# Kernel optimization log

Hardware: AMD Instinct MI355X
Metric: run time of the kernel (lower is better)

The kernel has to match this reference:

```python
import jax, jax.numpy as jnp
import numpy as np

# ---- quantization constants (8-bit, per-tensor affine; representative values) ----
Q_MAX = 255.0
S_IN, Z_IN = 0.05, 128.0      # block input
S1, Z1 = 0.04, 128.0          # after expand 1x1 + hardswish
S2, Z2 = 0.04, 128.0          # after depthwise 5x5 + hardswish
S_SE1, Z_SE1 = 0.03, 128.0    # SE fc1 output
S_SE2, Z_SE2 = 1.0 / 255.0, 0.0  # SE fc2 hardsigmoid output in [0,1]
S_MUL, Z_MUL = 0.04, 128.0    # SE gated activation
S3, Z3 = 0.05, 128.0          # after project 1x1
S_OUT, Z_OUT = 0.06, 128.0    # after residual add
W_SCALE = 0.01                # symmetric per-tensor weight scale (zero_point = 0)
EXP_C = 576                   # expanded channels (depthwise groups)


def conv(x, w, stride=1, padding=0, groups=1):
    return jax.lax.conv_general_dilated(
        x, w, (stride, stride), [(padding, padding), (padding, padding)],
        feature_group_count=groups, dimension_numbers=('NCHW', 'OIHW', 'NCHW'))


def hardswish(x):
    return x * jnp.clip(x + 3.0, 0.0, 6.0) * (1.0 / 6.0)


def hardsigmoid(x):
    return jnp.clip(x + 3.0, 0.0, 6.0) * (1.0 / 6.0)


def qconv(x_q, w_q, b_q, s_in, z_in, s_out, z_out, stride=1, padding=0, groups=1, act=None):
    """Quantized conv: int-domain accumulation (simulated in fp32), fused activation
    on the dequantized accumulator, then requantize to [0, Q_MAX]."""
    acc = conv(x_q - z_in, w_q, stride, padding, groups) + b_q[None, :, None, None]
    deq = acc * (s_in * W_SCALE)  # dequantize accumulator
    if act == 'hardswish':
        deq = hardswish(deq)
    elif act == 'hardsigmoid':
        deq = hardsigmoid(deq)
    return jnp.clip(deq * (1.0 / s_out) + z_out, 0.0, Q_MAX)


def setup_inputs() -> dict:
    key = jax.random.key(0)
    ks = jax.random.split(key, 11)
    def qw(k, shape):  # int8-style symmetric weights stored as fp32 integers
        return jnp.round(jnp.clip(jax.random.normal(k, shape) * 40.0, -127.0, 127.0))
    def qb(k, n):      # int32-style bias in accumulator domain
        return jnp.round(jax.random.normal(k, (n,)) * 500.0)
    return {
        'x':      jnp.round(jax.random.uniform(ks[0], (64, 96, 28, 28)) * Q_MAX),
        'w_exp':  qw(ks[1], (576, 96, 1, 1)),  'b_exp':  qb(ks[2], 576),
        'w_dw':   qw(ks[3], (576, 1, 5, 5)),   'b_dw':   qb(ks[4], 576),
        'w_se1':  qw(ks[5], (144, 576, 1, 1)), 'b_se1':  qb(ks[6], 144),
        'w_se2':  qw(ks[7], (576, 144, 1, 1)), 'b_se2':  qb(ks[8], 576),
        'w_proj': qw(ks[9], (96, 576, 1, 1)),  'b_proj': qb(ks[10], 96),
    }


def reference(x, w_exp, b_exp, w_dw, b_dw, w_se1, b_se1, w_se2, b_se2, w_proj, b_proj):
    # expand 1x1 (+ hardswish)
    e = qconv(x, w_exp, b_exp, S_IN, Z_IN, S1, Z1, act='hardswish')
    # depthwise 5x5, padding=(5-1)//2=2, groups=expanded (+ hardswish)
    d = qconv(e, w_dw, b_dw, S1, Z1, S2, Z2, padding=2, groups=EXP_C, act='hardswish')
    # squeeze-excitation: global avg pool -> fc1 -> fc2(hardsigmoid) -> quantized mul
    pooled = jnp.mean(d, axis=(2, 3), keepdims=True)  # [N, 576, 1, 1]
    g1 = qconv(pooled, w_se1, b_se1, S2, Z2, S_SE1, Z_SE1)
    g2 = qconv(g1, w_se2, b_se2, S_SE1, Z_SE1, S_SE2, Z_SE2, act='hardsigmoid')
    gated = jnp.clip((g2 - Z_SE2) * (d - Z2) * (S_SE2 * S2 / S_MUL) + Z_MUL, 0.0, Q_MAX)
    # project 1x1 (linear)
    p = qconv(gated, w_proj, b_proj, S_MUL, Z_MUL, S3, Z3)
    # quantized residual add (stride=1, in==out channels -> use_res_connect)
    out = jnp.clip((x - Z_IN) * (S_IN / S_OUT) + (p - Z3) * (S3 / S_OUT) + Z_OUT, 0.0, Q_MAX)
    return out
```

## Files before the change

### kernel.cpp

```cpp
#include <hip/hip_runtime.h>

typedef _Float16 v8h __attribute__((ext_vector_type(8)));
typedef _Float16 v4h __attribute__((ext_vector_type(4)));
typedef _Float16 v2h __attribute__((ext_vector_type(2)));
typedef float v4f __attribute__((ext_vector_type(4)));

#define NB 64
#define CI 96
#define CE 576
#define CO 96
#define HW 784
#define SEC 144

#if defined(__has_builtin)
#if __has_builtin(__builtin_amdgcn_fdot2)
#define HAVE_FDOT2 1
#endif
#endif

__device__ __forceinline__ float fdot2(v2h a, v2h b, float c) {
#ifdef HAVE_FDOT2
  return __builtin_amdgcn_fdot2(a, b, c, false);
#else
  return (float)a[0] * (float)b[0] + ((float)a[1] * (float)b[1] + c);
#endif
}

__global__ __launch_bounds__(256) void k0x_pack(const float* __restrict__ x,
                                                const float* __restrict__ w_exp,
                                                const float* __restrict__ w_proj,
                                                _Float16* __restrict__ x_f,
                                                _Float16* __restrict__ x_h,
                                                _Float16* __restrict__ w_exp_h,
                                                _Float16* __restrict__ w_proj_h) {
  __shared__ _Float16 xl[112][104];
  const int tid = threadIdx.x;
  const int n = blockIdx.y;
  const int hw0 = blockIdx.x * 112;

  if (n == 0) {
    for (int i = blockIdx.x * 256 + tid; i < CE * CI; i += 7 * 256) {
      w_exp_h[i]  = (_Float16)w_exp[i];
      w_proj_h[i] = (_Float16)w_proj[i];
    }
  }

  for (int idx = tid; idx < CI * 28; idx += 256) {
    int c = idx / 28, seg = idx % 28;
    const float4 v = *(const float4*)&x[(n * CI + c) * HW + hw0 + seg * 4];
    int row = seg * 4;
    v4h xh;
    xh[0] = (_Float16)(v.x - 128.0f);
    xh[1] = (_Float16)(v.y - 128.0f);
    xh[2] = (_Float16)(v.z - 128.0f);
    xh[3] = (_Float16)(v.w - 128.0f);
    xl[row + 0][c] = xh[0];
    xl[row + 1][c] = xh[1];
    xl[row + 2][c] = xh[2];
    xl[row + 3][c] = xh[3];
    *(v4h*)&x_h[(n * CI + c) * HW + hw0 + seg * 4] = xh;
  }
  __syncthreads();

  for (int idx = tid; idx < 1344; idx += 256) {
    int t_l = idx / 192, rem = idx % 192, s = rem / 64, ln = rem % 64;
    int hw_l = t_l * 16 + (ln & 15), ci = s * 32 + (ln >> 4) * 8;
    v8h o;
#pragma unroll
    for (int j = 0; j < 8; ++j) o[j] = xl[hw_l][ci + j];
    size_t t = (size_t)(blockIdx.x * 7 + t_l);
    *(v8h*)&x_f[(((size_t)n * 49 + t) * 3 + s) * 512 + ln * 8] = o;
  }
}

__global__ __launch_bounds__(512, 8) void k12_fused(const _Float16* __restrict__ x_f,
                                                    const _Float16* __restrict__ w_exp_h,
                                                    const float* __restrict__ b_exp,
                                                    const float* __restrict__ w_dw,
                                                    const float* __restrict__ b_dw,
                                                    _Float16* __restrict__ d_t,
                                                    float* __restrict__ d_sums2) {
  __shared__ _Float16 e_lds[16][18][42];
  __shared__ _Float16 d_tile[16][392];
  __shared__ _Float16 w_pairs[16][5][8];
  const int tid = threadIdx.x;
  const int n = blockIdx.z;
  const int h = blockIdx.y;
  const int c0 = blockIdx.x * 16;

  {
    unsigned long long* z = (unsigned long long*)&e_lds[0][0][0];
    for (int idx = tid; idx < 16 * 18 * 42 * 2 / 8; idx += 512) z[idx] = 0ull;
  }
  for (int idx = tid; idx < 640; idx += 512) {
    int c = idx / 40, r = idx % 40, dy = r / 8, k = r % 8;
    int tap = (k < 4) ? k : (k - 3);
    w_pairs[c][dy][k] = (_Float16)w_dw[(c0 + c) * 25 + dy * 5 + tap];
  }
  __syncthreads();

  const int wv = tid >> 6, lane = tid & 63;
  const int l15 = lane & 15, q = lane >> 4;

  {
    const _Float16* wrow = &w_exp_h[(c0 + l15) * CI + q * 8];
    v8h b0 = *(const v8h*)(wrow);
    v8h b1 = *(const v8h*)(wrow + 32);
    v8h b2 = *(const v8h*)(wrow + 64);
    const float bia = b_exp[c0 + l15];

    const int ir0 = 14 * h - 2;
    const _Float16* xb = x_f + (size_t)n * (49 * 3 * 512) + lane * 8;
    for (int t_l = wv; t_l < 28; t_l += 8) {
      int t = 21 * h + t_l;
      const _Float16* xt = xb + (size_t)t * (3 * 512);
      v8h a0 = *(const v8h*)(xt);
      v8h a1 = *(const v8h*)(xt + 512);
      v8h a2 = *(const v8h*)(xt + 1024);
      v4f acc = (v4f){0.f, 0.f, 0.f, 0.f};
      acc = __builtin_amdgcn_mfma_f32_16x16x32_f16(a0, b0, acc, 0, 0, 0);
      acc = __builtin_amdgcn_mfma_f32_16x16x32_f16(a1, b1, acc, 0, 0, 0);
      acc = __builtin_amdgcn_mfma_f32_16x16x32_f16(a2, b2, acc, 0, 0, 0);
      int p = t * 16 + q * 4;
      int y = p / 28, xx = p - y * 28;
      int r_l = y - ir0;
      v4h ev;
#pragma unroll
      for (int r = 0; r < 4; ++r) {
        float deq = (acc[r] + bia) * 5.0e-4f;
        float cl  = fminf(fmaxf(deq + 3.0f, 0.0f), 6.0f);
        float evf = fminf(fmaxf(deq * cl * (25.0f / 6.0f), -128.0f), 127.0f);
        ev[r] = (_Float16)evf;
      }
      *(v4h*)&e_lds[l15][r_l][8 + xx] = ev;
    }
  }
  __syncthreads();

  const int c = tid >> 5, l = tid & 31;
  v2h W01[5], W23[5], W12[5], W34[5];
  float W0s[5], W4s[5];
#pragma unroll
  for (int dy = 0; dy < 5; ++dy) {
    W01[dy] = *(const v2h*)&w_pairs[c][dy][0];
    W23[dy] = *(const v2h*)&w_pairs[c][dy][2];
    W12[dy] = *(const v2h*)&w_pairs[c][dy][4];
    W34[dy] = *(const v2h*)&w_pairs[c][dy][6];
    W0s[dy] = (float)W01[dy][0];
    W4s[dy] = (float)W34[dy][1];
  }
  const float bc = b_dw[c0 + c];

  float csum = 0.0f;
  if (l < 28) {
    const int ry = l >> 1;
    const int bx = (l & 1) * 14;
    v2h P0[5], P1[5], P2[5], P3[5];
#pragma unroll
    for (int dy = 0; dy < 5; ++dy) {
      const _Float16* row = &e_lds[c][ry + dy][bx];
      P0[dy] = *(const v2h*)(row + 6);
      P1[dy] = *(const v2h*)(row + 8);
      P2[dy] = *(const v2h*)(row + 10);
      P3[dy] = *(const v2h*)(row + 12);
    }
#pragma unroll
    for (int xi = 0; xi < 3; ++xi) {
      const int x0 = bx + xi * 4;
      float o0 = bc, o1 = bc, o2 = bc, o3 = bc;
#pragma unroll
      for (int dy = 0; dy < 5; ++dy) {
        o0 = fdot2(P0[dy], W01[dy], o0);
        o0 = fdot2(P1[dy], W23[dy], o0);
        o0 += (float)P2[dy][0] * W4s[dy];
        o1 += (float)P0[dy][1] * W0s[dy];
        o1 = fdot2(P1[dy], W12[dy], o1);
        o1 = fdot2(P2[dy], W34[dy], o1);
        o2 = fdot2(P1[dy], W01[dy], o2);
        o2 = fdot2(P2[dy], W23[dy], o2);
        o2 += (float)P3[dy][0] * W4s[dy];
        o3 += (float)P1[dy][1] * W0s[dy];
        o3 = fdot2(P2[dy], W12[dy], o3);
        o3 = fdot2(P3[dy], W34[dy], o3);
      }
      float oo[4] = {o0, o1, o2, o3};
      v2h dva, dvb;
#pragma unroll
      for (int i = 0; i < 4; ++i) {
        float deq = oo[i] * 4.0e-4f;
        float cl  = fminf(fmaxf(deq + 3.0f, 0.0f), 6.0f);
        float dvv = fminf(fmaxf(deq * cl * (25.0f / 6.0f), -128.0f), 127.0f);
        if (i < 2) dva[i] = (_Float16)dvv; else dvb[i - 2] = (_Float16)dvv;
        csum += dvv;
      }
      *(v2h*)&d_tile[c][ry * 28 + x0]     = dva;
      *(v2h*)&d_tile[c][ry * 28 + x0 + 2] = dvb;
#pragma unroll
      for (int dy = 0; dy < 5; ++dy) {
        const _Float16* row = &e_lds[c][ry + dy][bx];
        P0[dy] = P2[dy];
        P1[dy] = P3[dy];
        P2[dy] = *(const v2h*)(row + x0 - bx + 14);
        P3[dy] = *(const v2h*)(row + x0 - bx + 16);
      }
    }
    {
      float o0 = bc, o1 = bc;
#pragma unroll
      for (int dy = 0; dy < 5; ++dy) {
        o0 = fdot2(P0[dy], W01[dy], o0);
        o0 = fdot2(P1[dy], W23[dy], o0);
        o0 += (float)P2[dy][0] * W4s[dy];
        o1 += (float)P0[dy][1] * W0s[dy];
        o1 = fdot2(P1[dy], W12[dy], o1);
        o1 = fdot2(P2[dy], W34[dy], o1);
      }
      v2h dv;
      float oo[2] = {o0, o1};
#pragma unroll
      for (int i = 0; i < 2; ++i) {
        float deq = oo[i] * 4.0e-4f;
        float cl  = fminf(fmaxf(deq + 3.0f, 0.0f), 6.0f);
        float dvv = fminf(fmaxf(deq * cl * (25.0f / 6.0f), -128.0f), 127.0f);
        dv[i] = (_Float16)dvv;
        csum += dvv;
      }
      *(v2h*)&d_tile[c][ry * 28 + bx + 12] = dv;
    }
  }
#pragma unroll
  for (int m = 16; m >= 1; m >>= 1) csum += __shfl_xor(csum, m);
  if (l == 0) d_sums2[((size_t)h * NB + n) * CE + c0 + c] = csum;

  __syncthreads();
  const size_t obase = ((size_t)n * 72 + (c0 >> 3)) * 784 + 392 * h;
  if (tid < 392) {
    int hw_l = tid;
    v8h o0, o1;
#pragma unroll
    for (int j = 0; j < 8; ++j) { o0[j] = d_tile[j][hw_l]; o1[j] = d_tile[8 + j][hw_l]; }
    *(v8h*)&d_t[(obase + hw_l) * 8] = o0;
    *(v8h*)&d_t[(obase + 784 + hw_l) * 8] = o1;
  }
}

__global__ __launch_bounds__(256) void k3a_fc1(const float* __restrict__ d_sums2,
                                               const float* __restrict__ w_se1,
                                               const float* __restrict__ b_se1,
                                               float* __restrict__ g1) {
  const int tid = threadIdx.x;
  const int wv = tid >> 6, lane = tid & 63;
  const int n = blockIdx.y;
  const int o = blockIdx.x * 4 + wv;
  const float* wrow = &w_se1[o * CE];
  const float* s0 = &d_sums2[(size_t)n * CE];
  const float* s1 = &d_sums2[((size_t)NB + n) * CE];
  float p = 0.f;
#pragma unroll
  for (int s = 0; s < 9; ++s) {
    int cc = lane + s * 64;
    p += wrow[cc] * (s0[cc] + s1[cc]);
  }
#pragma unroll
  for (int m = 32; m >= 1; m >>= 1) p += __shfl_xor(p, m);
  if (lane == 0) {
    float deq = (p * (1.0f / 784.0f) + b_se1[o]) * 4.0e-4f;
    g1[n * SEC + o] = fminf(fmaxf(deq * 33.3333333f + 128.0f, 0.0f), 255.0f) - 128.0f;
  }
}

__global__ __launch_bounds__(256) void k3b_fc2(const float* __restrict__ g1,
                                               const float* __restrict__ w_se2,
                                               const float* __restrict__ b_se2,
                                               _Float16* __restrict__ g2h) {
  const int tid = threadIdx.x;
  const int wv = tid >> 6, lane = tid & 63;
  const int n = blockIdx.y;
  const int o = blockIdx.x * 4 + wv;
  const float* wrow = &w_se2[o * SEC];
  const float* grow = &g1[n * SEC];
  float p = wrow[lane] * grow[lane] + wrow[lane + 64] * grow[lane + 64];
  if (lane < 16) p += wrow[lane + 128] * grow[lane + 128];
#pragma unroll
  for (int m = 32; m >= 1; m >>= 1) p += __shfl_xor(p, m);
  if (lane == 0) {
    float deq = (p + b_se2[o]) * 3.0e-4f;
    g2h[n * CE + o] =
        (_Float16)(fminf(fmaxf(deq + 3.0f, 0.0f), 6.0f) * (1.0f / 6.0f));
  }
}

__global__ __launch_bounds__(192) void k4_proj(const _Float16* __restrict__ d_t,
                                               const _Float16* __restrict__ g2h,
                                               const _Float16* __restrict__ w_proj_h,
                                               const float* __restrict__ b_proj,
                                               const _Float16* __restrict__ x_h,
                                               float* __restrict__ out) {
  const int tid = threadIdx.x;
  const int n = blockIdx.z;
  const int co0 = blockIdx.y * 48;
  const int hw0 = blockIdx.x * 112;
  const int wv = tid >> 6, lane = tid & 63;
  const int l15 = lane & 15, q = lane >> 4;

  v4f acc[7];
#pragma unroll
  for (int t = 0; t < 7; ++t) acc[t] = (v4f){0.f, 0.f, 0.f, 0.f};

  const _Float16* dbase = d_t + (((size_t)n * 72 + q) * 784 + hw0 + l15) * 8;
  const _Float16* abase = &w_proj_h[(co0 + wv * 16 + l15) * CE + q * 8];
  const _Float16* gbase = &g2h[(size_t)n * CE + q * 8];

  for (int ks = 0; ks < 18; ++ks) {
    v8h a = *(const v8h*)(abase + ks * 32);
    v8h g = *(const v8h*)(gbase + ks * 32);
    v8h ag = a * g;
    const _Float16* dk = dbase + (size_t)ks * (4 * 784 * 8);
#pragma unroll
    for (int t = 0; t < 7; ++t) {
      v8h b = *(const v8h*)(dk + t * (16 * 8));
      acc[t] = __builtin_amdgcn_mfma_f32_16x16x32_f16(ag, b, acc[t], 0, 0, 0);
    }
  }

  float bia[4];
#pragma unroll
  for (int r = 0; r < 4; ++r) bia[r] = b_proj[co0 + wv * 16 + q * 4 + r];

#pragma unroll
  for (int t = 0; t < 7; ++t) {
#pragma unroll
    for (int r = 0; r < 4; ++r) {
      int co = co0 + wv * 16 + q * 4 + r;
      int hw = hw0 + t * 16 + l15;
      float p = fminf(fmaxf((acc[t][r] + bia[r]) * 4.0e-4f * 20.0f + 128.0f, 0.0f), 255.0f);
      float xv = (float)x_h[(n * CO + co) * HW + hw];
      float o = xv * 0.8333333333f + (p - 128.0f) * 0.8333333333f + 128.0f;
      out[(n * CO + co) * HW + hw] = fminf(fmaxf(o, 0.0f), 255.0f);
    }
  }
}

extern "C" void kernel_launch(void* const* d_in, const int* in_sizes, int n_in,
                              void* d_out, int out_size, void* d_ws, size_t ws_size,
                              hipStream_t stream) {
  const float* x      = (const float*)d_in[0];
  const float* w_exp  = (const float*)d_in[1];
  const float* b_exp  = (const float*)d_in[2];
  const float* w_dw   = (const float*)d_in[3];
  const float* b_dw   = (const float*)d_in[4];
  const float* w_se1  = (const float*)d_in[5];
  const float* b_se1  = (const float*)d_in[6];
  const float* w_se2  = (const float*)d_in[7];
  const float* b_se2  = (const float*)d_in[8];
  const float* w_proj = (const float*)d_in[9];
  const float* b_proj = (const float*)d_in[10];
  float* out = (float*)d_out;

  char* ws = (char*)d_ws;
  const size_t SZ_W  = (size_t)CE * CI * 2;
  const size_t SZ_XF = (size_t)NB * 49 * 3 * 512 * 2;
  const size_t SZ_XH = (size_t)NB * CI * HW * 2;
  const size_t SZ_D  = (size_t)NB * CE * HW * 2;
  const size_t SZ_S2 = (size_t)2 * NB * CE * 4;
  const size_t SZ_S  = (size_t)NB * CE * 4;
  _Float16* w_exp_h  = (_Float16*)(ws);
  _Float16* w_proj_h = (_Float16*)(ws + SZ_W);
  _Float16* x_f      = (_Float16*)(ws + 2 * SZ_W);
  _Float16* x_h      = (_Float16*)(ws + 2 * SZ_W + SZ_XF);
  _Float16* d_t      = (_Float16*)(ws + 2 * SZ_W + SZ_XF + SZ_XH);
  float*    d_sums2  = (float*)   (ws + 2 * SZ_W + SZ_XF + SZ_XH + SZ_D);
  float*    g1       = (float*)   (ws + 2 * SZ_W + SZ_XF + SZ_XH + SZ_D + SZ_S2);
  _Float16* g2h      = (_Float16*)(ws + 2 * SZ_W + SZ_XF + SZ_XH + SZ_D + SZ_S2 + SZ_S);

  k0x_pack<<<dim3(7, NB), 256, 0, stream>>>(x, w_exp, w_proj, x_f, x_h, w_exp_h, w_proj_h);
  k12_fused<<<dim3(36, 2, NB), 512, 0, stream>>>(x_f, w_exp_h, b_exp, w_dw, b_dw, d_t, d_sums2);
  k3a_fc1<<<dim3(36, NB), 256, 0, stream>>>(d_sums2, w_se1, b_se1, g1);
  k3b_fc2<<<dim3(144, NB), 256, 0, stream>>>(g1, w_se2, b_se2, g2h);
  k4_proj<<<dim3(7, 2, NB), 192, 0, stream>>>(d_t, g2h, w_proj_h, b_proj, x_h, out);
}
```

Before: 177.7 us.

## Split pack kernel by channel group and shrink fused kernel to 448 threads

The pack kernel now launches one block per 32-channel slice, so each block uses a smaller LDS tile and builds each fragment with a single vector LDS read. The fused expand+depthwise kernel drops from 512 to 448 threads: the MFMA loop is unrolled to exactly four tiles per wave, and the depthwise stage maps 28 threads per channel so no lanes sit idle. Because a channel's 28 threads no longer line up with a 32-lane group, the per-channel sum is now reduced through shared memory by 16 threads in the store phase. This adds an LDS array and a serial 28-element loop in exchange for fewer idle lanes and more pack parallelism.

```diff
diff --git a/kernel.cpp b/kernel.cpp
--- a/kernel.cpp
+++ b/kernel.cpp
@@ -33,47 +33,47 @@
                                                 _Float16* __restrict__ x_h,
                                                 _Float16* __restrict__ w_exp_h,
                                                 _Float16* __restrict__ w_proj_h) {
-  __shared__ _Float16 xl[112][104];
-  const int tid = threadIdx.x;
-  const int n = blockIdx.y;
+  __shared__ _Float16 xl[112][40];
+  const int tid = threadIdx.x;
+  const int s = blockIdx.y;
+  const int n = blockIdx.z;
   const int hw0 = blockIdx.x * 112;
 
-  if (n == 0) {
+  if (n == 0 && s == 0) {
     for (int i = blockIdx.x * 256 + tid; i < CE * CI; i += 7 * 256) {
       w_exp_h[i]  = (_Float16)w_exp[i];
       w_proj_h[i] = (_Float16)w_proj[i];
     }
   }
 
-  for (int idx = tid; idx < CI * 28; idx += 256) {
-    int c = idx / 28, seg = idx % 28;
+  for (int idx = tid; idx < 32 * 28; idx += 256) {
+    int c_l = idx / 28, seg = idx % 28;
+    int c = s * 32 + c_l;
     const float4 v = *(const float4*)&x[(n * CI + c) * HW + hw0 + seg * 4];
-    int row = seg * 4;
     v4h xh;
     xh[0] = (_Float16)(v.x - 128.0f);
     xh[1] = (_Float16)(v.y - 128.0f);
     xh[2] = (_Float16)(v.z - 128.0f);
     xh[3] = (_Float16)(v.w - 128.0f);
-    xl[row + 0][c] = xh[0];
-    xl[row + 1][c] = xh[1];
-    xl[row + 2][c] = xh[2];
-    xl[row + 3][c] = xh[3];
+    int row = seg * 4;
+    xl[row + 0][c_l] = xh[0];
+    xl[row + 1][c_l] = xh[1];
+    xl[row + 2][c_l] = xh[2];
+    xl[row + 3][c_l] = xh[3];
     *(v4h*)&x_h[(n * CI + c) * HW + hw0 + seg * 4] = xh;
   }
   __syncthreads();
 
-  for (int idx = tid; idx < 1344; idx += 256) {
-    int t_l = idx / 192, rem = idx % 192, s = rem / 64, ln = rem % 64;
-    int hw_l = t_l * 16 + (ln & 15), ci = s * 32 + (ln >> 4) * 8;
-    v8h o;
-#pragma unroll
-    for (int j = 0; j < 8; ++j) o[j] = xl[hw_l][ci + j];
+  for (int idx = tid; idx < 448; idx += 256) {
+    int t_l = idx / 64, ln = idx % 64;
+    int hw_l = t_l * 16 + (ln & 15), ci = (ln >> 4) * 8;
+    v8h o = *(const v8h*)&xl[hw_l][ci];
     size_t t = (size_t)(blockIdx.x * 7 + t_l);
     *(v8h*)&x_f[(((size_t)n * 49 + t) * 3 + s) * 512 + ln * 8] = o;
   }
 }
 
-__global__ __launch_bounds__(512, 8) void k12_fused(const _Float16* __restrict__ x_f,
+__global__ __launch_bounds__(448, 7) void k12_fused(const _Float16* __restrict__ x_f,
                                                     const _Float16* __restrict__ w_exp_h,
                                                     const float* __restrict__ b_exp,
                                                     const float* __restrict__ w_dw,
@@ -83,6 +83,7 @@
   __shared__ _Float16 e_lds[16][18][42];
   __shared__ _Float16 d_tile[16][392];
   __shared__ _Float16 w_pairs[16][5][8];
+  __shared__ float red[448];
   const int tid = threadIdx.x;
   const int n = blockIdx.z;
   const int h = blockIdx.y;
@@ -90,9 +91,9 @@
 
   {
     unsigned long long* z = (unsigned long long*)&e_lds[0][0][0];
-    for (int idx = tid; idx < 16 * 18 * 42 * 2 / 8; idx += 512) z[idx] = 0ull;
-  }
-  for (int idx = tid; idx < 640; idx += 512) {
+    for (int idx = tid; idx < 16 * 18 * 42 * 2 / 8; idx += 448) z[idx] = 0ull;
+  }
+  for (int idx = tid; idx < 640; idx += 448) {
     int c = idx / 40, r = idx % 40, dy = r / 8, k = r % 8;
     int tap = (k < 4) ? k : (k - 3);
     w_pairs[c][dy][k] = (_Float16)w_dw[(c0 + c) * 25 + dy * 5 + tap];
@@ -111,7 +112,9 @@
 
     const int ir0 = 14 * h - 2;
     const _Float16* xb = x_f + (size_t)n * (49 * 3 * 512) + lane * 8;
-    for (int t_l = wv; t_l < 28; t_l += 8) {
+#pragma unroll
+    for (int i = 0; i < 4; ++i) {
+      int t_l = wv + 7 * i;
       int t = 21 * h + t_l;
       const _Float16* xt = xb + (size_t)t * (3 * 512);
       v8h a0 = *(const v8h*)(xt);
@@ -137,7 +140,7 @@
   }
   __syncthreads();
 
-  const int c = tid >> 5, l = tid & 31;
+  const int c = tid / 28, l = tid % 28;
   v2h W01[5], W23[5], W12[5], W34[5];
   float W0s[5], W4s[5];
 #pragma unroll
@@ -152,7 +155,7 @@
   const float bc = b_dw[c0 + c];
 
   float csum = 0.0f;
-  if (l < 28) {
+  {
     const int ry = l >> 1;
     const int bx = (l & 1) * 14;
     v2h P0[5], P1[5], P2[5], P3[5];
@@ -228,19 +231,23 @@
       *(v2h*)&d_tile[c][ry * 28 + bx + 12] = dv;
     }
   }
-#pragma unroll
-  for (int m = 16; m >= 1; m >>= 1) csum += __shfl_xor(csum, m);
-  if (l == 0) d_sums2[((size_t)h * NB + n) * CE + c0 + c] = csum;
-
+  red[tid] = csum;
   __syncthreads();
-  const size_t obase = ((size_t)n * 72 + (c0 >> 3)) * 784 + 392 * h;
+
   if (tid < 392) {
     int hw_l = tid;
+    const size_t obase = ((size_t)n * 72 + (c0 >> 3)) * 784 + 392 * h;
     v8h o0, o1;
 #pragma unroll
     for (int j = 0; j < 8; ++j) { o0[j] = d_tile[j][hw_l]; o1[j] = d_tile[8 + j][hw_l]; }
     *(v8h*)&d_t[(obase + hw_l) * 8] = o0;
     *(v8h*)&d_t[(obase + 784 + hw_l) * 8] = o1;
+  } else if (tid < 408) {
+    int cc = tid - 392;
+    float s = 0.f;
+#pragma unroll
+    for (int k = 0; k < 28; ++k) s += red[cc * 28 + k];
+    d_sums2[((size_t)h * NB + n) * CE + c0 + cc] = s;
   }
 }
 
@@ -373,8 +380,8 @@
   float*    g1       = (float*)   (ws + 2 * SZ_W + SZ_XF + SZ_XH + SZ_D + SZ_S2);
   _Float16* g2h      = (_Float16*)(ws + 2 * SZ_W + SZ_XF + SZ_XH + SZ_D + SZ_S2 + SZ_S);
 
-  k0x_pack<<<dim3(7, NB), 256, 0, stream>>>(x, w_exp, w_proj, x_f, x_h, w_exp_h, w_proj_h);
-  k12_fused<<<dim3(36, 2, NB), 512, 0, stream>>>(x_f, w_exp_h, b_exp, w_dw, b_dw, d_t, d_sums2);
+  k0x_pack<<<dim3(7, 3, NB), 256, 0, stream>>>(x, w_exp, w_proj, x_f, x_h, w_exp_h, w_proj_h);
+  k12_fused<<<dim3(36, 2, NB), 448, 0, stream>>>(x_f, w_exp_h, b_exp, w_dw, b_dw, d_t, d_sums2);
   k3a_fc1<<<dim3(36, NB), 256, 0, stream>>>(d_sums2, w_se1, b_se1, g1);
   k3b_fc2<<<dim3(144, NB), 256, 0, stream>>>(g1, w_se2, b_se2, g2h);
   k4_proj<<<dim3(7, 2, NB), 192, 0, stream>>>(d_t, g2h, w_proj_h, b_proj, x_h, out);
```

After: 178.8 us. Within noise of the previous version (+0.7%).
